# Kernel tuning notes

Hardware: AMD Instinct MI355X
Metric: run time of the kernel (lower is better)

Reference implementation:

```python
import jax, jax.numpy as jnp
import numpy as np

EPS = 1e-7  # K.epsilon()


def setup_inputs() -> dict:
    key = jax.random.key(0)
    k1, k2, k3 = jax.random.split(key, 3)
    B, T, D = 64, 2048, 256
    x = jax.random.normal(k1, (B, T, D), dtype=jnp.float32)
    W = jax.random.normal(k2, (D, D), dtype=jnp.float32) * (1.0 / np.sqrt(D))
    b = jnp.zeros((D,), dtype=jnp.float32)
    uw = jax.random.normal(k3, (D,), dtype=jnp.float32) * (1.0 / np.sqrt(D))
    mask = jnp.ones((B, T), dtype=jnp.int32)
    return {"x": x, "W": W, "b": b, "uw": uw, "mask": mask}


def reference(x, W, b, uw, mask):
    # x: [B, T, D]; W: [D, D]; b, uw: [D]; mask: [B, T]
    eij = jnp.tanh(jnp.einsum('btd,de->bte', x, W) + b)   # [B, T, D]
    eij = jnp.einsum('btd,d->bt', eij, uw)                # [B, T]
    a = jnp.exp(eij) * mask.astype(x.dtype)               # [B, T]
    a = a / (jnp.sum(a, axis=1, keepdims=True) + EPS)     # normalize over time
    return jnp.einsum('btd,bt->bd', x, a)                 # [B, D]
```

## Files before the change

### kernel.cpp

```cpp
#include <hip/hip_runtime.h>
#include <hip/hip_bf16.h>

#define BB 64
#define TT 2048
#define DD 256
#define EPSF 1e-7f
#define XS_STRIDE 264

typedef __attribute__((ext_vector_type(8))) short v8s;
typedef __attribute__((ext_vector_type(4))) float v4f;

__device__ __forceinline__ float bf2f(unsigned short u) {
    union { unsigned int i; float f; } c;
    c.i = ((unsigned int)u) << 16;
    return c.f;
}

__device__ __forceinline__ unsigned int pack2_bf16(float a, float b) {
    union { __hip_bfloat162 h; unsigned int u; } c;
    c.h = __float22bfloat162_rn(make_float2(a, b));
    return c.u;
}

__device__ __forceinline__ float tanh_fast(float x) {
    float e = __expf(2.0f * x);
    return 1.0f - 2.0f / (e + 1.0f);
}

__global__ __launch_bounds__(256) void pack_wt(const float* __restrict__ W,
                                               unsigned short* __restrict__ Wt) {
    __shared__ float tile[32][33];
    int bx = blockIdx.x & 7;
    int by = blockIdx.x >> 3;
    int r  = threadIdx.x >> 3;
    int c4 = (threadIdx.x & 7) * 4;
    float4 v = *(const float4*)(W + (size_t)(bx * 32 + r) * DD + by * 32 + c4);
    tile[r][c4 + 0] = v.x; tile[r][c4 + 1] = v.y;
    tile[r][c4 + 2] = v.z; tile[r][c4 + 3] = v.w;
    __syncthreads();
    float a0 = tile[c4 + 0][r], a1 = tile[c4 + 1][r];
    float a2 = tile[c4 + 2][r], a3 = tile[c4 + 3][r];
    uint2 pp = make_uint2(pack2_bf16(a0, a1), pack2_bf16(a2, a3));
    *(uint2*)(Wt + (size_t)(by * 32 + r) * DD + bx * 32 + c4) = pp;
}

__global__ __launch_bounds__(256, 3) void fused_att3(const float* __restrict__ x,
                                                     const unsigned short* __restrict__ Wt,
                                                     const float* __restrict__ bias,
                                                     const float* __restrict__ uw,
                                                     const int* __restrict__ mask,
                                                     float* __restrict__ numpart,
                                                     float* __restrict__ denpart) {
    __shared__ unsigned short xs[64 * XS_STRIDE];
    __shared__ float ered[4][64];
    __shared__ float red[4][DD];
    __shared__ float denred[4];

    const int tid  = threadIdx.x;
    const int w    = tid >> 6;
    const int lane = tid & 63;
    const int quad = lane >> 4;
    const int m    = lane & 15;
    const long R0  = (long)blockIdx.x * 64 + w * 16;

    float bias_r[4], uw_r[4];
#pragma unroll
    for (int i = 0; i < 4; ++i) {
        int n = (w * 4 + i) * 16 + m;
        bias_r[i] = bias[n];
        uw_r[i]   = uw[n];
    }

    {
        const float* gp = x + R0 * DD + lane * 4;
        unsigned short* sp = xs + (size_t)(w * 16) * XS_STRIDE + lane * 4;
#pragma unroll 8
        for (int r = 0; r < 16; ++r) {
            float4 v = *(const float4*)(gp + (size_t)r * DD);
            uint2 pp = make_uint2(pack2_bf16(v.x, v.y), pack2_bf16(v.z, v.w));
            *(uint2*)(sp + (size_t)r * XS_STRIDE) = pp;
        }
    }
    __syncthreads();

    float esum[4][4];
#pragma unroll
    for (int mt = 0; mt < 4; ++mt)
#pragma unroll
        for (int r = 0; r < 4; ++r) esum[mt][r] = 0.f;

#pragma unroll
    for (int h = 0; h < 2; ++h) {
        v8s a0[8], a1[8];
        {
            const unsigned short* ap0 = xs + (size_t)(2 * h * 16 + m) * XS_STRIDE + quad * 8;
#pragma unroll
            for (int ks = 0; ks < 8; ++ks) {
                a0[ks] = *(const v8s*)(ap0 + ks * 32);
                a1[ks] = *(const v8s*)(ap0 + 16 * XS_STRIDE + ks * 32);
            }
        }
        v8s bbuf[2][8];
        {
            const unsigned short* bp = Wt + (size_t)(w * 4 * 16 + m) * DD + quad * 8;
#pragma unroll
            for (int ks = 0; ks < 8; ++ks) bbuf[0][ks] = *(const v8s*)(bp + ks * 32);
        }
#pragma unroll
        for (int i = 0; i < 4; ++i) {
            const int cur = i & 1;
            if (i < 3) {
                const unsigned short* bp = Wt + (size_t)((w * 4 + i + 1) * 16 + m) * DD + quad * 8;
#pragma unroll
                for (int ks = 0; ks < 8; ++ks) bbuf[cur ^ 1][ks] = *(const v8s*)(bp + ks * 32);
            }
            v4f acc0 = {0.f, 0.f, 0.f, 0.f};
            v4f acc1 = {0.f, 0.f, 0.f, 0.f};
#pragma unroll
            for (int ks = 0; ks < 8; ++ks) {
                acc0 = __builtin_amdgcn_mfma_f32_16x16x32_bf16(a0[ks], bbuf[cur][ks], acc0, 0, 0, 0);
                acc1 = __builtin_amdgcn_mfma_f32_16x16x32_bf16(a1[ks], bbuf[cur][ks], acc1, 0, 0, 0);
            }
#pragma unroll
            for (int r = 0; r < 4; ++r) {
                esum[2 * h][r]     += tanh_fast(acc0[r] + bias_r[i]) * uw_r[i];
                esum[2 * h + 1][r] += tanh_fast(acc1[r] + bias_r[i]) * uw_r[i];
            }
        }
    }

#pragma unroll
    for (int o = 1; o < 16; o <<= 1)
#pragma unroll
        for (int mt = 0; mt < 4; ++mt)
#pragma unroll
            for (int r = 0; r < 4; ++r)
                esum[mt][r] += __shfl_xor(esum[mt][r], o, 64);
    if (m == 0) {
#pragma unroll
        for (int mt = 0; mt < 4; ++mt)
#pragma unroll
            for (int r = 0; r < 4; ++r)
                ered[w][mt * 16 + quad * 4 + r] = esum[mt][r];
    }
    __syncthreads();

    const int rl = lane & 15;
    float et = ered[0][w * 16 + rl] + ered[1][w * 16 + rl]
             + ered[2][w * 16 + rl] + ered[3][w * 16 + rl];
    float p_loc = __expf(et) * (float)mask[R0 + rl];
    float p_all[16];
#pragma unroll
    for (int t = 0; t < 16; ++t) p_all[t] = __shfl(p_loc, t, 64);
    float den = 0.f;
#pragma unroll
    for (int t = 0; t < 16; ++t) den += p_all[t];

    float num[4] = {0.f, 0.f, 0.f, 0.f};
    {
        const unsigned short* xp = xs + (size_t)(w * 16) * XS_STRIDE + lane * 4;
#pragma unroll
        for (int t = 0; t < 16; ++t) {
            uint2 xv = *(const uint2*)(xp + (size_t)t * XS_STRIDE);
            float pt = p_all[t];
            num[0] += pt * bf2f((unsigned short)(xv.x & 0xffffu));
            num[1] += pt * bf2f((unsigned short)(xv.x >> 16));
            num[2] += pt * bf2f((unsigned short)(xv.y & 0xffffu));
            num[3] += pt * bf2f((unsigned short)(xv.y >> 16));
        }
    }

    *(float4*)&red[w][lane * 4] = make_float4(num[0], num[1], num[2], num[3]);
    if (lane == 0) denred[w] = den;
    __syncthreads();
    float s = red[0][tid] + red[1][tid] + red[2][tid] + red[3][tid];
    numpart[(size_t)blockIdx.x * DD + tid] = s;
    if (tid == 0) denpart[blockIdx.x] = denred[0] + denred[1] + denred[2] + denred[3];
}

__global__ __launch_bounds__(256) void finalize(const float* __restrict__ numpart,
                                                const float* __restrict__ denpart,
                                                float* __restrict__ out) {
    __shared__ float dsh;
    int b = blockIdx.x, d = threadIdx.x;
    if (d == 0) {
        float s = 0.f;
        for (int c = 0; c < 32; ++c) s += denpart[b * 32 + c];
        dsh = s + EPSF;
    }
    __syncthreads();
    float s = 0.f;
#pragma unroll
    for (int c = 0; c < 32; ++c) s += numpart[(size_t)(b * 32 + c) * DD + d];
    out[(size_t)b * DD + d] = s / dsh;
}

extern "C" void kernel_launch(void* const* d_in, const int* in_sizes, int n_in,
                              void* d_out, int out_size, void* d_ws, size_t ws_size,
                              hipStream_t stream) {
    const float* x    = (const float*)d_in[0];
    const float* W    = (const float*)d_in[1];
    const float* bias = (const float*)d_in[2];
    const float* uw   = (const float*)d_in[3];
    const int*   mask = (const int*)d_in[4];
    float*       out  = (float*)d_out;

    char* ws = (char*)d_ws;
    unsigned short* Wt = (unsigned short*)ws;
    float* numpart     = (float*)(ws + 131072);
    float* denpart     = (float*)(ws + 131072 + 2097152);

    pack_wt<<<dim3(64), dim3(256), 0, stream>>>(W, Wt);
    fused_att3<<<dim3(2048), dim3(256), 0, stream>>>(x, Wt, bias, uw, mask, numpart, denpart);
    finalize<<<dim3(64), dim3(256), 0, stream>>>(numpart, denpart, out);
}
```

Measured before the change: 231.1 us.

## Halve rows per block to 32 and raise occupancy to six blocks per CU

The fused attention kernel now handles 32 time rows per block instead of 64, launching 4096 blocks with launch bounds allowing 6 blocks per CU. Shared memory and the register footprint shrink, which should let more waves run at once and hide the memory latency of streaming x. The denominator is now reduced with a wavefront shuffle instead of a shared-memory pass. The finalize kernel is rewritten to sum 64 partials per batch using float4 loads split across four thread groups. The cost is twice as many W tile loads per row processed and a larger partial-sum buffer to reduce.

Result: slower. 256.0 us (+10.8%).

```diff
diff --git a/kernel.cpp b/kernel.cpp
--- a/kernel.cpp
+++ b/kernel.cpp
@@ -5,6 +5,7 @@
 #define TT 2048
 #define DD 256
 #define EPSF 1e-7f
+#define ROWS 32
 #define XS_STRIDE 264
 
 typedef __attribute__((ext_vector_type(8))) short v8s;
@@ -44,24 +45,24 @@
     *(uint2*)(Wt + (size_t)(by * 32 + r) * DD + bx * 32 + c4) = pp;
 }
 
-__global__ __launch_bounds__(256, 3) void fused_att3(const float* __restrict__ x,
+__global__ __launch_bounds__(256, 6) void fused_att4(const float* __restrict__ x,
                                                      const unsigned short* __restrict__ Wt,
                                                      const float* __restrict__ bias,
                                                      const float* __restrict__ uw,
                                                      const int* __restrict__ mask,
                                                      float* __restrict__ numpart,
                                                      float* __restrict__ denpart) {
-    __shared__ unsigned short xs[64 * XS_STRIDE];
-    __shared__ float ered[4][64];
+    __shared__ unsigned short xs[ROWS * XS_STRIDE];
+    __shared__ float ered[4][ROWS];
     __shared__ float red[4][DD];
-    __shared__ float denred[4];
 
     const int tid  = threadIdx.x;
     const int w    = tid >> 6;
     const int lane = tid & 63;
     const int quad = lane >> 4;
     const int m    = lane & 15;
-    const long R0  = (long)blockIdx.x * 64 + w * 16;
+    const long R0  = (long)blockIdx.x * ROWS;
+    const long Rw  = R0 + w * 8;
 
     float bias_r[4], uw_r[4];
 #pragma unroll
@@ -72,10 +73,10 @@
     }
 
     {
-        const float* gp = x + R0 * DD + lane * 4;
-        unsigned short* sp = xs + (size_t)(w * 16) * XS_STRIDE + lane * 4;
-#pragma unroll 8
-        for (int r = 0; r < 16; ++r) {
+        const float* gp = x + Rw * DD + lane * 4;
+        unsigned short* sp = xs + (size_t)(w * 8) * XS_STRIDE + lane * 4;
+#pragma unroll
+        for (int r = 0; r < 8; ++r) {
             float4 v = *(const float4*)(gp + (size_t)r * DD);
             uint2 pp = make_uint2(pack2_bf16(v.x, v.y), pack2_bf16(v.z, v.w));
             *(uint2*)(sp + (size_t)r * XS_STRIDE) = pp;
@@ -83,84 +84,81 @@
     }
     __syncthreads();
 
-    float esum[4][4];
-#pragma unroll
-    for (int mt = 0; mt < 4; ++mt)
+    float esum[2][4];
+#pragma unroll
+    for (int mt = 0; mt < 2; ++mt)
 #pragma unroll
         for (int r = 0; r < 4; ++r) esum[mt][r] = 0.f;
 
-#pragma unroll
-    for (int h = 0; h < 2; ++h) {
-        v8s a0[8], a1[8];
-        {
-            const unsigned short* ap0 = xs + (size_t)(2 * h * 16 + m) * XS_STRIDE + quad * 8;
-#pragma unroll
-            for (int ks = 0; ks < 8; ++ks) {
-                a0[ks] = *(const v8s*)(ap0 + ks * 32);
-                a1[ks] = *(const v8s*)(ap0 + 16 * XS_STRIDE + ks * 32);
-            }
-        }
-        v8s bbuf[2][8];
-        {
-            const unsigned short* bp = Wt + (size_t)(w * 4 * 16 + m) * DD + quad * 8;
-#pragma unroll
-            for (int ks = 0; ks < 8; ++ks) bbuf[0][ks] = *(const v8s*)(bp + ks * 32);
-        }
-#pragma unroll
-        for (int i = 0; i < 4; ++i) {
-            const int cur = i & 1;
-            if (i < 3) {
-                const unsigned short* bp = Wt + (size_t)((w * 4 + i + 1) * 16 + m) * DD + quad * 8;
-#pragma unroll
-                for (int ks = 0; ks < 8; ++ks) bbuf[cur ^ 1][ks] = *(const v8s*)(bp + ks * 32);
-            }
-            v4f acc0 = {0.f, 0.f, 0.f, 0.f};
-            v4f acc1 = {0.f, 0.f, 0.f, 0.f};
-#pragma unroll
-            for (int ks = 0; ks < 8; ++ks) {
-                acc0 = __builtin_amdgcn_mfma_f32_16x16x32_bf16(a0[ks], bbuf[cur][ks], acc0, 0, 0, 0);
-                acc1 = __builtin_amdgcn_mfma_f32_16x16x32_bf16(a1[ks], bbuf[cur][ks], acc1, 0, 0, 0);
-            }
-#pragma unroll
-            for (int r = 0; r < 4; ++r) {
-                esum[2 * h][r]     += tanh_fast(acc0[r] + bias_r[i]) * uw_r[i];
-                esum[2 * h + 1][r] += tanh_fast(acc1[r] + bias_r[i]) * uw_r[i];
-            }
+    v8s a0[8], a1[8];
+    {
+        const unsigned short* ap0 = xs + (size_t)m * XS_STRIDE + quad * 8;
+#pragma unroll
+        for (int ks = 0; ks < 8; ++ks) {
+            a0[ks] = *(const v8s*)(ap0 + ks * 32);
+            a1[ks] = *(const v8s*)(ap0 + 16 * XS_STRIDE + ks * 32);
+        }
+    }
+    v8s bbuf[2][8];
+    {
+        const unsigned short* bp = Wt + (size_t)(w * 64 + m) * DD + quad * 8;
+#pragma unroll
+        for (int ks = 0; ks < 8; ++ks) bbuf[0][ks] = *(const v8s*)(bp + ks * 32);
+    }
+#pragma unroll
+    for (int i = 0; i < 4; ++i) {
+        const int cur = i & 1;
+        if (i < 3) {
+            const unsigned short* bp = Wt + (size_t)((w * 4 + i + 1) * 16 + m) * DD + quad * 8;
+#pragma unroll
+            for (int ks = 0; ks < 8; ++ks) bbuf[cur ^ 1][ks] = *(const v8s*)(bp + ks * 32);
+        }
+        v4f acc0 = {0.f, 0.f, 0.f, 0.f};
+        v4f acc1 = {0.f, 0.f, 0.f, 0.f};
+#pragma unroll
+        for (int ks = 0; ks < 8; ++ks) {
+            acc0 = __builtin_amdgcn_mfma_f32_16x16x32_bf16(a0[ks], bbuf[cur][ks], acc0, 0, 0, 0);
+            acc1 = __builtin_amdgcn_mfma_f32_16x16x32_bf16(a1[ks], bbuf[cur][ks], acc1, 0, 0, 0);
+        }
+#pragma unroll
+        for (int r = 0; r < 4; ++r) {
+            esum[0][r] += tanh_fast(acc0[r] + bias_r[i]) * uw_r[i];
+            esum[1][r] += tanh_fast(acc1[r] + bias_r[i]) * uw_r[i];
         }
     }
 
 #pragma unroll
     for (int o = 1; o < 16; o <<= 1)
 #pragma unroll
-        for (int mt = 0; mt < 4; ++mt)
+        for (int mt = 0; mt < 2; ++mt)
 #pragma unroll
             for (int r = 0; r < 4; ++r)
                 esum[mt][r] += __shfl_xor(esum[mt][r], o, 64);
     if (m == 0) {
 #pragma unroll
-        for (int mt = 0; mt < 4; ++mt)
+        for (int mt = 0; mt < 2; ++mt)
 #pragma unroll
             for (int r = 0; r < 4; ++r)
                 ered[w][mt * 16 + quad * 4 + r] = esum[mt][r];
     }
     __syncthreads();
 
-    const int rl = lane & 15;
-    float et = ered[0][w * 16 + rl] + ered[1][w * 16 + rl]
-             + ered[2][w * 16 + rl] + ered[3][w * 16 + rl];
+    const int rl = lane & 31;
+    float et = ered[0][rl] + ered[1][rl] + ered[2][rl] + ered[3][rl];
     float p_loc = __expf(et) * (float)mask[R0 + rl];
-    float p_all[16];
-#pragma unroll
-    for (int t = 0; t < 16; ++t) p_all[t] = __shfl(p_loc, t, 64);
-    float den = 0.f;
-#pragma unroll
-    for (int t = 0; t < 16; ++t) den += p_all[t];
+    float den = p_loc;
+#pragma unroll
+    for (int o = 1; o < 32; o <<= 1) den += __shfl_xor(den, o, 64);
+
+    float p_all[8];
+#pragma unroll
+    for (int t = 0; t < 8; ++t) p_all[t] = __shfl(p_loc, w * 8 + t, 64);
 
     float num[4] = {0.f, 0.f, 0.f, 0.f};
     {
-        const unsigned short* xp = xs + (size_t)(w * 16) * XS_STRIDE + lane * 4;
-#pragma unroll
-        for (int t = 0; t < 16; ++t) {
+        const unsigned short* xp = xs + (size_t)(w * 8) * XS_STRIDE + lane * 4;
+#pragma unroll
+        for (int t = 0; t < 8; ++t) {
             uint2 xv = *(const uint2*)(xp + (size_t)t * XS_STRIDE);
             float pt = p_all[t];
             num[0] += pt * bf2f((unsigned short)(xv.x & 0xffffu));
@@ -171,28 +169,41 @@
     }
 
     *(float4*)&red[w][lane * 4] = make_float4(num[0], num[1], num[2], num[3]);
-    if (lane == 0) denred[w] = den;
     __syncthreads();
     float s = red[0][tid] + red[1][tid] + red[2][tid] + red[3][tid];
     numpart[(size_t)blockIdx.x * DD + tid] = s;
-    if (tid == 0) denpart[blockIdx.x] = denred[0] + denred[1] + denred[2] + denred[3];
+    if (tid == 0) denpart[blockIdx.x] = den;
 }
 
 __global__ __launch_bounds__(256) void finalize(const float* __restrict__ numpart,
                                                 const float* __restrict__ denpart,
                                                 float* __restrict__ out) {
-    __shared__ float dsh;
-    int b = blockIdx.x, d = threadIdx.x;
-    if (d == 0) {
-        float s = 0.f;
-        for (int c = 0; c < 32; ++c) s += denpart[b * 32 + c];
-        dsh = s + EPSF;
-    }
-    __syncthreads();
-    float s = 0.f;
-#pragma unroll
-    for (int c = 0; c < 32; ++c) s += numpart[(size_t)(b * 32 + c) * DD + d];
-    out[(size_t)b * DD + d] = s / dsh;
+    __shared__ float4 part[4][64];
+    int b = blockIdx.x, t = threadIdx.x;
+    int d4 = t & 63;
+    int cq = t >> 6;
+    float4 s = make_float4(0.f, 0.f, 0.f, 0.f);
+    const float* np = numpart + ((size_t)b * 64 + (size_t)cq * 16) * DD + d4 * 4;
+#pragma unroll
+    for (int c = 0; c < 16; ++c) {
+        float4 v = *(const float4*)(np + (size_t)c * DD);
+        s.x += v.x; s.y += v.y; s.z += v.z; s.w += v.w;
+    }
+    part[cq][d4] = s;
+    float dp = (t < 64) ? denpart[b * 64 + t] : 0.f;
+    __syncthreads();
+    if (t < 64) {
+#pragma unroll
+        for (int o = 1; o < 64; o <<= 1) dp += __shfl_xor(dp, o, 64);
+        float4 p0 = part[0][t], p1 = part[1][t], p2 = part[2][t], p3 = part[3][t];
+        float inv = 1.0f / (dp + EPSF);
+        float4 r;
+        r.x = (p0.x + p1.x + p2.x + p3.x) * inv;
+        r.y = (p0.y + p1.y + p2.y + p3.y) * inv;
+        r.z = (p0.z + p1.z + p2.z + p3.z) * inv;
+        r.w = (p0.w + p1.w + p2.w + p3.w) * inv;
+        *(float4*)(out + (size_t)b * DD + t * 4) = r;
+    }
 }
 
 extern "C" void kernel_launch(void* const* d_in, const int* in_sizes, int n_in,
@@ -208,9 +219,9 @@
     char* ws = (char*)d_ws;
     unsigned short* Wt = (unsigned short*)ws;
     float* numpart     = (float*)(ws + 131072);
-    float* denpart     = (float*)(ws + 131072 + 2097152);
+    float* denpart     = (float*)(ws + 131072 + 4194304);
 
     pack_wt<<<dim3(64), dim3(256), 0, stream>>>(W, Wt);
-    fused_att3<<<dim3(2048), dim3(256), 0, stream>>>(x, Wt, bias, uw, mask, numpart, denpart);
+    fused_att4<<<dim3(4096), dim3(256), 0, stream>>>(x, Wt, bias, uw, mask, numpart, denpart);
     finalize<<<dim3(64), dim3(256), 0, stream>>>(numpart, denpart, out);
 }
```
